# Performance work log

Hardware: AMD Instinct MI355X
Metric: run time of the kernel (lower is better)

## Reference

```python
import jax, jax.numpy as jnp
import numpy as np

DIM = 2048
HEAD_DIM = 64
NUM_HEADS = DIM // HEAD_DIM
ROT_DIM = HEAD_DIM // 2  # 32
THETA = 10000.0
LN_EPS = 1e-5


def setup_inputs() -> dict:
    key = jax.random.key(0)
    ks = jax.random.split(key, 6)
    n, s = 2, 2048
    x = jax.random.normal(ks[0], (n, s, DIM), dtype=jnp.float32)
    ln_w = jnp.ones((DIM,), dtype=jnp.float32)
    ln_b = jnp.zeros((DIM,), dtype=jnp.float32)
    # Linear weights stored as (in, out); torch Linear init scale ~ 1/sqrt(in)
    sc = 1.0 / np.sqrt(DIM)
    w_qkv = jax.random.uniform(ks[1], (DIM, 3 * DIM), jnp.float32, -sc, sc)
    b_qkv = jax.random.uniform(ks[2], (3 * DIM,), jnp.float32, -sc, sc)
    w_out = jax.random.uniform(ks[3], (DIM, DIM), jnp.float32, -sc, sc)
    b_out = jax.random.uniform(ks[4], (DIM,), jnp.float32, -sc, sc)
    return {"x": x, "ln_w": ln_w, "ln_b": ln_b, "w_qkv": w_qkv,
            "b_qkv": b_qkv, "w_out": w_out, "b_out": b_out}


def _rope_cos_sin(seq_len):
    # freqs: theta ** linspace(0, -1, rot_dim//2 + 1)[:-1] -> 16 freqs
    n_freq = ROT_DIM // 2
    exps = jnp.linspace(0.0, -1.0, n_freq + 1)[:-1]
    freqs = THETA ** exps  # [16]
    pos = jnp.arange(seq_len, dtype=jnp.float32)  # [s]
    tmp = pos[:, None] * freqs[None, :]  # [s, 16]
    # broadcast target: [1, 1, s, 16] over (n, h, s, d)
    return jnp.cos(tmp)[None, None], jnp.sin(tmp)[None, None]


def _apply_rotary(x, cos, sin):
    d = cos.shape[-1]  # 16
    x1, x2, x3 = x[..., :d], x[..., d:2 * d], x[..., 2 * d:]
    y1 = x1 * cos - x2 * sin
    y2 = x2 * cos + x1 * sin
    return jnp.concatenate([y1.astype(x3.dtype), y2.astype(x3.dtype), x3], axis=-1)


def reference(x, ln_w, ln_b, w_qkv, b_qkv, w_out, b_out):
    n, s, dim = x.shape
    skip = x
    # LayerNorm
    mu = jnp.mean(x, axis=-1, keepdims=True)
    var = jnp.var(x, axis=-1, keepdims=True)
    h = (x - mu) * jax.lax.rsqrt(var + LN_EPS) * ln_w + ln_b
    # fused QKV projection
    qkv = h @ w_qkv + b_qkv  # [n, s, 3*dim]
    qkv = qkv.reshape(n, s, 3, NUM_HEADS, HEAD_DIM)
    qkv = jnp.transpose(qkv, (2, 0, 3, 1, 4))  # [3, n, h, s, d]
    q, k, v = qkv[0], qkv[1], qkv[2]
    # RoPE on first rot_dim dims
    cos, sin = _rope_cos_sin(s)
    q = _apply_rotary(q, cos, sin)
    k = _apply_rotary(k, cos, sin)
    # causal SDPA
    scale = 1.0 / jnp.sqrt(jnp.asarray(HEAD_DIM, dtype=q.dtype))
    scores = jnp.einsum('nhqd,nhkd->nhqk', q, k) * scale
    causal = jnp.tril(jnp.ones((s, s), dtype=bool))
    scores = jnp.where(causal[None, None], scores, jnp.asarray(-jnp.inf, scores.dtype))
    attn = jax.nn.softmax(scores, axis=-1)
    o = jnp.einsum('nhqk,nhkd->nhqd', attn, v)  # [n, h, s, d]
    o = jnp.transpose(o, (0, 2, 1, 3)).reshape(n, s, dim)
    return o @ w_out + b_out + skip
```

## Files before the change

### kernel.cpp

```cpp
#include <hip/hip_runtime.h>
#include <hip/hip_bf16.h>
#include <cstdint>
#include <cstddef>

#define DIMM 2048
#define NHEADS 32
#define HDIM 64
#define SEQ 2048
#define NBATCH 2
#define ROWS 4096
#define NFREQ 16
#define NKT 64

typedef __bf16 bfv8 __attribute__((ext_vector_type(8)));
typedef float f32x4v __attribute__((ext_vector_type(4)));
typedef float f32x16 __attribute__((ext_vector_type(16)));

__device__ __forceinline__ void gload16(const void* g, void* l) {
  __builtin_amdgcn_global_load_lds((const __attribute__((address_space(1))) void*)g,
                                   (__attribute__((address_space(3))) void*)l, 16, 0, 0);
}

__device__ __forceinline__ f32x4v mfma16(bfv8 a, bfv8 b, f32x4v c) {
  return __builtin_amdgcn_mfma_f32_16x16x32_bf16(a, b, c, 0, 0, 0);
}

__device__ __forceinline__ f32x16 mfma32(bfv8 a, bfv8 b, f32x16 c) {
  return __builtin_amdgcn_mfma_f32_32x32x16_bf16(a, b, c, 0, 0, 0);
}

__device__ __forceinline__ unsigned short f2bfu(float f) {
  __hip_bfloat16 h = __float2bfloat16(f);
  return __builtin_bit_cast(unsigned short, h);
}

__device__ __forceinline__ unsigned pack2bf(float a, float b) {
  return (unsigned)f2bfu(a) | ((unsigned)f2bfu(b) << 16);
}

__device__ __forceinline__ void swap32(unsigned& a, unsigned& b, const int hi) {
  const unsigned ta = (unsigned)__shfl_xor((int)a, 32);
  const unsigned tb = (unsigned)__shfl_xor((int)b, 32);
  const unsigned na = hi ? tb : a;
  const unsigned nb = hi ? b : ta;
  a = na;
  b = nb;
}

__device__ __forceinline__ void xcd_swizzle(int& bx, int& by) {
  const int gx = gridDim.x, nwg = gx * gridDim.y;
  const int orig = blockIdx.y * gx + blockIdx.x;
  const int q = nwg >> 3, r = nwg & 7;
  const int xcd = orig & 7, loc = orig >> 3;
  const int wg = (xcd < r ? xcd * (q + 1) : r * (q + 1) + (xcd - r) * q) + loc;
  bx = wg % gx;
  by = wg / gx;
}

__global__ __launch_bounds__(256) void rope_tab_kernel(float* __restrict__ ct,
                                                       float* __restrict__ st) {
  const int i = blockIdx.x * 256 + threadIdx.x;
  if (i >= SEQ * NFREQ) return;
  const int pos = i >> 4, f = i & 15;
  const float freq = powf(10000.0f, -(float)f / 16.0f);
  const float ang = (float)pos * freq;
  ct[i] = cosf(ang);
  st[i] = sinf(ang);
}

__global__ __launch_bounds__(256) void transpose_cast_kernel(const float* __restrict__ W,
                                                             __hip_bfloat16* __restrict__ WT,
                                                             int K, int N) {
  __shared__ float tile[32][33];
  const int n0 = blockIdx.x * 32, k0 = blockIdx.y * 32;
  const int tx = threadIdx.x, ty = threadIdx.y;
#pragma unroll
  for (int j = 0; j < 4; ++j)
    tile[ty + j * 8][tx] = W[(size_t)(k0 + ty + j * 8) * N + n0 + tx];
  __syncthreads();
#pragma unroll
  for (int j = 0; j < 4; ++j)
    WT[(size_t)(n0 + ty + j * 8) * K + k0 + tx] = __float2bfloat16(tile[tx][ty + j * 8]);
}

__global__ __launch_bounds__(256) void ln_kernel(const float* __restrict__ x,
                                                 const float* __restrict__ lw,
                                                 const float* __restrict__ lb,
                                                 __hip_bfloat16* __restrict__ h) {
  const int row = blockIdx.x;
  const int t = threadIdx.x;
  const float4* xr = (const float4*)(x + (size_t)row * DIMM);
  float4 a = xr[t * 2], b = xr[t * 2 + 1];
  float e[8];
  *(float4*)e = a; *(float4*)(e + 4) = b;
  float s = 0.f, ss = 0.f;
#pragma unroll
  for (int j = 0; j < 8; ++j) { s += e[j]; ss += e[j] * e[j]; }
#pragma unroll
  for (int o = 1; o < 64; o <<= 1) { s += __shfl_xor(s, o); ss += __shfl_xor(ss, o); }
  __shared__ float red[8];
  const int wid = t >> 6;
  if ((t & 63) == 0) { red[wid * 2] = s; red[wid * 2 + 1] = ss; }
  __syncthreads();
  s = red[0] + red[2] + red[4] + red[6];
  ss = red[1] + red[3] + red[5] + red[7];
  const float mu = s * (1.f / DIMM);
  const float var = ss * (1.f / DIMM) - mu * mu;
  const float rs = rsqrtf(var + 1e-5f);
  const float4* w4 = (const float4*)lw;
  const float4* b4 = (const float4*)lb;
  float4 wa = w4[t * 2], wb = w4[t * 2 + 1], ba = b4[t * 2], bb = b4[t * 2 + 1];
  float wv[8], bv[8];
  *(float4*)wv = wa; *(float4*)(wv + 4) = wb;
  *(float4*)bv = ba; *(float4*)(bv + 4) = bb;
  unsigned short hv[8];
#pragma unroll
  for (int j = 0; j < 8; ++j)
    hv[j] = f2bfu((e[j] - mu) * rs * wv[j] + bv[j]);
  *(uint4*)((char*)h + (size_t)row * (DIMM * 2) + t * 16) = *(uint4*)hv;
}

__device__ __forceinline__ void stage_tile(const char* Ab, const char* Bb,
                                           int brow, int bcol, int kt, char* buf,
                                           int tid) {
  const int wid = tid >> 6, lane = tid & 63;
#pragma unroll
  for (int i = 0; i < 4; ++i) {
    const int fw = wid * 1024 + i * 4096;
    const int f = fw + lane * 16;
    const int lr = f >> 6;
    const int src = (f & 63) ^ (((lr >> 1) & 3) << 4);
    gload16(Ab + (size_t)(brow + lr) * 4096 + kt * 64 + src, buf + fw);
  }
#pragma unroll
  for (int i = 0; i < 2; ++i) {
    const int fw = wid * 1024 + i * 4096;
    const int f = fw + lane * 16;
    const int lr = f >> 6;
    const int src = (f & 63) ^ (((lr >> 1) & 3) << 4);
    gload16(Bb + (size_t)(bcol + lr) * 4096 + kt * 64 + src, buf + 16384 + fw);
  }
}

__device__ __forceinline__ void gemm_core(const char* Ab, const char* Bb,
                                          int brow, int bcol, char* lds,
                                          f32x4v acc[8][4]) {
  const int tid = threadIdx.x;
  const int lane = tid & 63, wid = tid >> 6;
  const int g = lane >> 4, ln15 = lane & 15;
  const int wr = wid >> 1, wc = wid & 1;
  stage_tile(Ab, Bb, brow, bcol, 0, lds, tid);
  stage_tile(Ab, Bb, brow, bcol, 1, lds + 24576, tid);
  asm volatile("s_waitcnt vmcnt(6)" ::: "memory");
  __syncthreads();
  for (int kt = 0; kt < NKT; ++kt) {
    char* buf = lds + (kt & 1) * 24576;
    bfv8 af[8], bfr[4];
#pragma unroll
    for (int mf = 0; mf < 8; ++mf) {
      const int ra = wr * 128 + mf * 16 + ln15;
      af[mf] = *(const bfv8*)(buf + ra * 64 + ((g * 16) ^ (((ra >> 1) & 3) << 4)));
    }
#pragma unroll
    for (int nf = 0; nf < 4; ++nf) {
      const int rb = wc * 64 + nf * 16 + ln15;
      bfr[nf] = *(const bfv8*)(buf + 16384 + rb * 64 + ((g * 16) ^ (((rb >> 1) & 3) << 4)));
    }
    asm volatile("s_waitcnt lgkmcnt(0)" ::: "memory");
    __builtin_amdgcn_sched_barrier(0);
    __syncthreads();
    if (kt + 2 < NKT) stage_tile(Ab, Bb, brow, bcol, kt + 2, buf, tid);
    __builtin_amdgcn_s_setprio(1);
#pragma unroll
    for (int mf = 0; mf < 8; ++mf)
#pragma unroll
      for (int nf = 0; nf < 4; ++nf)
        acc[mf][nf] = mfma16(af[mf], bfr[nf], acc[mf][nf]);
    __builtin_amdgcn_s_setprio(0);
    if (kt + 2 < NKT) {
      asm volatile("s_waitcnt vmcnt(6)" ::: "memory");
    } else {
      asm volatile("s_waitcnt vmcnt(0)" ::: "memory");
    }
    __syncthreads();
  }
}

__global__ __launch_bounds__(256, 2) void gemm_qkv_kernel(
    const __hip_bfloat16* __restrict__ A, const __hip_bfloat16* __restrict__ BT,
    const float* __restrict__ bqkv, const float* __restrict__ ct, const float* __restrict__ st,
    __hip_bfloat16* __restrict__ qb, __hip_bfloat16* __restrict__ kb,
    __hip_bfloat16* __restrict__ vb) {
  __shared__ char lds[49152];
  const f32x4v fz = {0.f, 0.f, 0.f, 0.f};
  f32x4v acc[8][4];
#pragma unroll
  for (int mf = 0; mf < 8; ++mf)
#pragma unroll
    for (int nf = 0; nf < 4; ++nf) acc[mf][nf] = fz;
  int bx, by;
  xcd_swizzle(bx, by);
  const int brow = by * 256, bcol = bx * 128;
  gemm_core((const char*)A, (const char*)BT, brow, bcol, lds, acc);

  const int tid = threadIdx.x, lane = tid & 63, wid = tid >> 6;
  const int g = lane >> 4, ln15 = lane & 15;
  const int wr = wid >> 1, wc = wid & 1;
  const int cb = bcol + wc * 64;
  const int which = cb >> 11;
  const int head = (cb & 2047) >> 6;
  float bias[4];
#pragma unroll
  for (int nf = 0; nf < 4; ++nf) bias[nf] = bqkv[cb + nf * 16 + ln15];

  if (which == 2) {
    char* tp = lds + wid * 8192;
    const int nidx = brow >> 11;
    const size_t vhead = ((size_t)nidx * NHEADS + head) * (HDIM * SEQ);
#pragma unroll
    for (int hm = 0; hm < 2; ++hm) {
      if (hm == 1) {
        asm volatile("s_waitcnt lgkmcnt(0)" ::: "memory");
        __builtin_amdgcn_sched_barrier(0);
      }
#pragma unroll
      for (int mf4 = 0; mf4 < 4; ++mf4)
#pragma unroll
        for (int r = 0; r < 4; ++r) {
          const int mf = hm * 4 + mf4;
          const int posl = mf4 * 16 + g * 4 + r;
#pragma unroll
          for (int nf = 0; nf < 4; ++nf) {
            const int d = nf * 16 + ln15;
            *(unsigned short*)(tp + d * 128 + ((posl * 2) ^ ((d & 7) << 4))) =
                f2bfu(acc[mf][nf][r] + bias[nf]);
          }
        }
      asm volatile("s_waitcnt lgkmcnt(0)" ::: "memory");
      __builtin_amdgcn_sched_barrier(0);
      const int posb = (brow & 2047) + wr * 128 + hm * 64;
#pragma unroll
      for (int i = 0; i < 8; ++i) {
        const int dl = i * 8 + (lane >> 3);
        const int cs = (lane & 7) ^ (dl & 7);
        const uint4 val = *(const uint4*)(tp + dl * 128 + cs * 16);
        *(uint4*)((char*)vb + (vhead + (size_t)dl * SEQ + posb + (lane & 7) * 8) * 2) = val;
      }
    }
  } else {
    __hip_bfloat16* dst = (which == 0) ? qb : kb;
#pragma unroll
    for (int mf = 0; mf < 8; ++mf)
#pragma unroll
      for (int r = 0; r < 4; ++r) {
        const int row = brow + wr * 128 + mf * 16 + g * 4 + r;
        const int nidx = row >> 11, pos = row & 2047;
        float v0 = acc[mf][0][r] + bias[0];
        float v1 = acc[mf][1][r] + bias[1];
        float v2 = acc[mf][2][r] + bias[2];
        float v3 = acc[mf][3][r] + bias[3];
        const float c0 = ct[pos * 16 + ln15], s0 = st[pos * 16 + ln15];
        const float x1 = v0, x2 = v1;
        v0 = x1 * c0 - x2 * s0;
        v1 = x2 * c0 + x1 * s0;
        __hip_bfloat16* p = dst + (((size_t)(nidx * NHEADS + head)) * SEQ + pos) * HDIM;
        p[ln15] = __float2bfloat16(v0);
        p[16 + ln15] = __float2bfloat16(v1);
        p[32 + ln15] = __float2bfloat16(v2);
        p[48 + ln15] = __float2bfloat16(v3);
      }
  }
}

__global__ __launch_bounds__(256, 2) void gemm_out_kernel(
    const __hip_bfloat16* __restrict__ A, const __hip_bfloat16* __restrict__ BT,
    const float* __restrict__ bout, const float* __restrict__ skip,
    float* __restrict__ out) {
  __shared__ char lds[49152];
  const f32x4v fz = {0.f, 0.f, 0.f, 0.f};
  f32x4v acc[8][4];
#pragma unroll
  for (int mf = 0; mf < 8; ++mf)
#pragma unroll
    for (int nf = 0; nf < 4; ++nf) acc[mf][nf] = fz;
  int bx, by;
  xcd_swizzle(bx, by);
  const int brow = by * 256, bcol = bx * 128;
  gemm_core((const char*)A, (const char*)BT, brow, bcol, lds, acc);

  const int tid = threadIdx.x, lane = tid & 63, wid = tid >> 6;
  const int g = lane >> 4, ln15 = lane & 15;
  const int wr = wid >> 1, wc = wid & 1;
#pragma unroll
  for (int mf = 0; mf < 8; ++mf)
#pragma unroll
    for (int r = 0; r < 4; ++r) {
      const int row = brow + wr * 128 + mf * 16 + g * 4 + r;
      const float* xr = skip + (size_t)row * DIMM;
      float* orow = out + (size_t)row * DIMM;
#pragma unroll
      for (int nf = 0; nf < 4; ++nf) {
        const int c = bcol + wc * 64 + nf * 16 + ln15;
        orow[c] = acc[mf][nf][r] + bout[c] + xr[c];
      }
    }
}

__global__ __launch_bounds__(256) void attn_kernel(
    const __hip_bfloat16* __restrict__ qb, const __hip_bfloat16* __restrict__ kb,
    const __hip_bfloat16* __restrict__ vtb, __hip_bfloat16* __restrict__ ob) {
  __shared__ char sm[33280];
  float* lred = (float*)(sm + 32768);
  const int tid = threadIdx.x, lane = tid & 63, wid = tid >> 6;
  const int ln31 = lane & 31, hi = lane >> 5;
  const int head = blockIdx.x;
  const int qbi = (int)gridDim.y - 1 - (int)blockIdx.y;
  const size_t hb = (size_t)head * (SEQ * HDIM);
  const int q0 = qbi * 128;
  const int qw = q0 + wid * 32;
  const int qg = qw + ln31;
  const int nt = qbi * 2 + 2;
  const char* Kg = (const char*)(kb + hb);
  const char* Vg = (const char*)(vtb + hb);

  bfv8 qf[4];
  {
    const char* Qp = (const char*)(qb + hb) + (size_t)(qw + ln31) * 128 + hi * 16;
#pragma unroll
    for (int j = 0; j < 4; ++j) qf[j] = *(const bfv8*)(Qp + j * 32);
  }

  f32x16 o0, o1;
#pragma unroll
  for (int i = 0; i < 16; ++i) { o0[i] = 0.f; o1[i] = 0.f; }
  float m_run = -1e30f, l_run = 0.f;
  const float scale = 0.125f;
  const int swz = (ln31 & 7) << 4;

#pragma unroll
  for (int i = 0; i < 2; ++i) {
    const int f = (tid + i * 256) * 16;
    const int row = f >> 7;
    const int src = (f & 127) ^ ((row & 7) << 4);
    gload16(Kg + (size_t)row * 128 + src, sm + f);
    gload16(Vg + (size_t)row * 4096 + src, sm + 16384 + f);
  }
  asm volatile("s_waitcnt vmcnt(0)" ::: "memory");
  __syncthreads();

  for (int t = 0; t < nt; ++t) {
    const int kvb = t * 64;
    if (t + 1 < nt) {
      const int nb = (t + 1) & 1;
      const int kvb2 = kvb + 64;
#pragma unroll
      for (int i = 0; i < 2; ++i) {
        const int f = (tid + i * 256) * 16;
        const int row = f >> 7;
        const int src = (f & 127) ^ ((row & 7) << 4);
        gload16(Kg + (size_t)(kvb2 + row) * 128 + src, sm + nb * 8192 + f);
        gload16(Vg + (size_t)row * 4096 + (size_t)kvb2 * 2 + src, sm + 16384 + nb * 8192 + f);
      }
    }
    if (kvb <= qw + 31) {
      const char* ldsK = sm + (t & 1) * 8192;
      const char* ldsV = sm + 16384 + (t & 1) * 8192;
      f32x16 s0, s1;
#pragma unroll
      for (int i = 0; i < 16; ++i) { s0[i] = 0.f; s1[i] = 0.f; }
      __builtin_amdgcn_s_setprio(1);
#pragma unroll
      for (int j = 0; j < 4; ++j) {
        const int byt = j * 32 + hi * 16;
        const bfv8 k0 = *(const bfv8*)(ldsK + ln31 * 128 + (byt ^ swz));
        const bfv8 k1 = *(const bfv8*)(ldsK + (32 + ln31) * 128 + (byt ^ swz));
        s0 = mfma32(k0, qf[j], s0);
        s1 = mfma32(k1, qf[j], s1);
      }
      __builtin_amdgcn_s_setprio(0);
      float p[32];
#pragma unroll
      for (int r = 0; r < 16; ++r) { p[r] = s0[r] * scale; p[16 + r] = s1[r] * scale; }
      if (kvb + 63 > qw) {
#pragma unroll
        for (int r = 0; r < 16; ++r) {
          const int kvo = (r & 3) + 8 * (r >> 2) + 4 * hi;
          if (kvb + kvo > qg) p[r] = -1e30f;
          if (kvb + 32 + kvo > qg) p[16 + r] = -1e30f;
        }
      }
      float mx = p[0];
#pragma unroll
      for (int r = 1; r < 32; ++r) mx = fmaxf(mx, p[r]);
      mx = fmaxf(mx, __shfl_xor(mx, 32));
      if (!__all(mx <= m_run + 8.0f)) {
        const float mn = fmaxf(m_run, mx);
        const float al = __expf(m_run - mn);
        m_run = mn;
        l_run *= al;
        lred[wid * 32 + ln31] = al;
        asm volatile("s_waitcnt lgkmcnt(0)" ::: "memory");
        __builtin_amdgcn_sched_barrier(0);
#pragma unroll
        for (int r = 0; r < 16; ++r) {
          const float a = lred[wid * 32 + (r & 3) + 8 * (r >> 2) + 4 * hi];
          o0[r] *= a;
          o1[r] *= a;
        }
      }
      float ps = 0.f;
#pragma unroll
      for (int r = 0; r < 32; ++r) { p[r] = __expf(p[r] - m_run); ps += p[r]; }
      ps += __shfl_xor(ps, 32);
      l_run += ps;
      unsigned c[16];
#pragma unroll
      for (int i = 0; i < 16; ++i) c[i] = pack2bf(p[2 * i], p[2 * i + 1]);
      bfv8 paf[4];
#pragma unroll
      for (int fI = 0; fI < 4; ++fI) {
        unsigned a0 = c[fI * 4 + 0], b0 = c[fI * 4 + 2];
        unsigned a1 = c[fI * 4 + 1], b1 = c[fI * 4 + 3];
        swap32(a0, b0, hi);
        swap32(a1, b1, hi);
        union { unsigned u[4]; bfv8 v; } w;
        w.u[0] = a0; w.u[1] = a1; w.u[2] = b0; w.u[3] = b1;
        paf[fI] = w.v;
      }
      __builtin_amdgcn_s_setprio(1);
#pragma unroll
      for (int ss = 0; ss < 4; ++ss) {
        const int byt = ss * 32 + hi * 16;
        const bfv8 v0 = *(const bfv8*)(ldsV + ln31 * 128 + (byt ^ swz));
        const bfv8 v1 = *(const bfv8*)(ldsV + (32 + ln31) * 128 + (byt ^ swz));
        o0 = mfma32(paf[ss], v0, o0);
        o1 = mfma32(paf[ss], v1, o1);
      }
      __builtin_amdgcn_s_setprio(0);
    }
    asm volatile("s_waitcnt vmcnt(0)" ::: "memory");
    __syncthreads();
  }

  lred[wid * 32 + ln31] = l_run;
  asm volatile("s_waitcnt lgkmcnt(0)" ::: "memory");
  __builtin_amdgcn_sched_barrier(0);
  const int nidx = head >> 5, hh = head & 31;
#pragma unroll
  for (int r = 0; r < 16; ++r) {
    const int qrow = qw + (r & 3) + 8 * (r >> 2) + 4 * hi;
    const float inv = 1.0f / lred[wid * 32 + (r & 3) + 8 * (r >> 2) + 4 * hi];
    __hip_bfloat16* dst = ob + ((size_t)nidx * SEQ + qrow) * DIMM + hh * 64;
    dst[ln31] = __float2bfloat16(o0[r] * inv);
    dst[32 + ln31] = __float2bfloat16(o1[r] * inv);
  }
}

extern "C" void kernel_launch(void* const* d_in, const int* in_sizes, int n_in,
                              void* d_out, int out_size, void* d_ws, size_t ws_size,
                              hipStream_t stream) {
  const float* x = (const float*)d_in[0];
  const float* ln_w = (const float*)d_in[1];
  const float* ln_b = (const float*)d_in[2];
  const float* w_qkv = (const float*)d_in[3];
  const float* b_qkv = (const float*)d_in[4];
  const float* w_out = (const float*)d_in[5];
  const float* b_out = (const float*)d_in[6];
  float* out = (float*)d_out;

  char* ws = (char*)d_ws;
  size_t off = 0;
  auto alloc = [&](size_t bytes) -> char* {
    char* p = ws + off;
    off += (bytes + 255) & ~(size_t)255;
    return p;
  };
  __hip_bfloat16* h = (__hip_bfloat16*)alloc((size_t)ROWS * DIMM * 2);
  __hip_bfloat16* wqkvT = (__hip_bfloat16*)alloc((size_t)3 * DIMM * DIMM * 2);
  __hip_bfloat16* woutT = (__hip_bfloat16*)alloc((size_t)DIMM * DIMM * 2);
  __hip_bfloat16* qbuf = (__hip_bfloat16*)alloc((size_t)ROWS * DIMM * 2);
  __hip_bfloat16* kbuf = (__hip_bfloat16*)alloc((size_t)ROWS * DIMM * 2);
  __hip_bfloat16* vtbuf = (__hip_bfloat16*)alloc((size_t)ROWS * DIMM * 2);
  __hip_bfloat16* obuf = (__hip_bfloat16*)alloc((size_t)ROWS * DIMM * 2);
  float* ct = (float*)alloc((size_t)SEQ * NFREQ * 4);
  float* st = (float*)alloc((size_t)SEQ * NFREQ * 4);

  rope_tab_kernel<<<dim3((SEQ * NFREQ + 255) / 256), dim3(256), 0, stream>>>(ct, st);
  transpose_cast_kernel<<<dim3(3 * DIMM / 32, DIMM / 32), dim3(32, 8), 0, stream>>>(
      w_qkv, wqkvT, DIMM, 3 * DIMM);
  transpose_cast_kernel<<<dim3(DIMM / 32, DIMM / 32), dim3(32, 8), 0, stream>>>(
      w_out, woutT, DIMM, DIMM);
  ln_kernel<<<dim3(ROWS), dim3(256), 0, stream>>>(x, ln_w, ln_b, h);
  gemm_qkv_kernel<<<dim3(3 * DIMM / 128, ROWS / 256), dim3(256), 0, stream>>>(
      h, wqkvT, b_qkv, ct, st, qbuf, kbuf, vtbuf);
  attn_kernel<<<dim3(NBATCH * NHEADS, SEQ / 128), dim3(256), 0, stream>>>(
      qbuf, kbuf, vtbuf, obuf);
  gemm_out_kernel<<<dim3(DIMM / 128, ROWS / 256), dim3(256), 0, stream>>>(
      obuf, woutT, b_out, x, out);
}
```

Baseline: 300.5 us.

## Restructure GEMMs to 8 waves with split-K, triple-buffered 128-wide K tiles

Both projection GEMMs now use 512 threads, with pairs of waves splitting each K tile of 128 in half. Partial accumulators are combined through LDS before the epilogue. The main loop uses a three-stage LDS ring and issues global loads in two chunks interleaved with two MFMA halves, with one barrier per iteration instead of two. This aims to hide memory latency and raise MFMA issue rate, at the cost of 144KB of LDS per block, which likely limits occupancy to one block per CU despite the launch bound of 2, plus an extra reduction pass.

```diff
diff --git a/kernel.cpp b/kernel.cpp
--- a/kernel.cpp
+++ b/kernel.cpp
@@ -10,7 +10,7 @@
 #define NBATCH 2
 #define ROWS 4096
 #define NFREQ 16
-#define NKT 64
+#define NKT3 32
 
 typedef __bf16 bfv8 __attribute__((ext_vector_type(8)));
 typedef float f32x4v __attribute__((ext_vector_type(4)));
@@ -120,78 +120,126 @@
   *(uint4*)((char*)h + (size_t)row * (DIMM * 2) + t * 16) = *(uint4*)hv;
 }
 
-__device__ __forceinline__ void stage_tile(const char* Ab, const char* Bb,
-                                           int brow, int bcol, int kt, char* buf,
-                                           int tid) {
-  const int wid = tid >> 6, lane = tid & 63;
-#pragma unroll
-  for (int i = 0; i < 4; ++i) {
-    const int fw = wid * 1024 + i * 4096;
-    const int f = fw + lane * 16;
-    const int lr = f >> 6;
-    const int src = (f & 63) ^ (((lr >> 1) & 3) << 4);
-    gload16(Ab + (size_t)(brow + lr) * 4096 + kt * 64 + src, buf + fw);
-  }
-#pragma unroll
-  for (int i = 0; i < 2; ++i) {
-    const int fw = wid * 1024 + i * 4096;
-    const int f = fw + lane * 16;
-    const int lr = f >> 6;
-    const int src = (f & 63) ^ (((lr >> 1) & 3) << 4);
-    gload16(Bb + (size_t)(bcol + lr) * 4096 + kt * 64 + src, buf + 16384 + fw);
-  }
-}
-
-__device__ __forceinline__ void gemm_core(const char* Ab, const char* Bb,
-                                          int brow, int bcol, char* lds,
-                                          f32x4v acc[8][4]) {
-  const int tid = threadIdx.x;
-  const int lane = tid & 63, wid = tid >> 6;
+__device__ __forceinline__ void stageA64(const char* Ab, int brow, int kt,
+                                         char* bufA, int c, int lane) {
+  const int row = c * 8 + (lane >> 3);
+  const int src = ((lane & 7) * 16) ^ ((row & 7) << 4);
+  gload16(Ab + (size_t)(brow + row) * 4096 + kt * 128 + src, bufA + c * 1024);
+}
+__device__ __forceinline__ void stageB64(const char* Bb, int bcol, int kt,
+                                         char* bufB, int c, int lane) {
+  const int row = c * 8 + (lane >> 3);
+  const int src = ((lane & 7) * 16) ^ ((row & 7) << 4);
+  gload16(Bb + (size_t)(bcol + row) * 4096 + kt * 128 + src, bufB + c * 1024);
+}
+
+__device__ __forceinline__ void gemm_core3(const char* Ab, const char* Bb,
+                                           int brow, int bcol, char* lds,
+                                           f32x4v acc[8][4]) {
+  const int tid = threadIdx.x, lane = tid & 63, wid = tid >> 6;
   const int g = lane >> 4, ln15 = lane & 15;
-  const int wr = wid >> 1, wc = wid & 1;
-  stage_tile(Ab, Bb, brow, bcol, 0, lds, tid);
-  stage_tile(Ab, Bb, brow, bcol, 1, lds + 24576, tid);
+  const int wr = wid >> 2, wc = (wid >> 1) & 1, wk = wid & 1;
+  const int kb = wk * 64;
+
+#pragma unroll
+  for (int t = 0; t < 2; ++t) {
+    char* bufA = lds + t * 49152;
+    char* bufB = bufA + 32768;
+    stageA64(Ab, brow, t, bufA, wid, lane);
+    stageA64(Ab, brow, t, bufA, wid + 8, lane);
+    stageA64(Ab, brow, t, bufA, wid + 16, lane);
+    stageA64(Ab, brow, t, bufA, wid + 24, lane);
+    stageB64(Bb, bcol, t, bufB, wid, lane);
+    stageB64(Bb, bcol, t, bufB, wid + 8, lane);
+  }
   asm volatile("s_waitcnt vmcnt(6)" ::: "memory");
-  __syncthreads();
-  for (int kt = 0; kt < NKT; ++kt) {
-    char* buf = lds + (kt & 1) * 24576;
-    bfv8 af[8], bfr[4];
-#pragma unroll
-    for (int mf = 0; mf < 8; ++mf) {
-      const int ra = wr * 128 + mf * 16 + ln15;
-      af[mf] = *(const bfv8*)(buf + ra * 64 + ((g * 16) ^ (((ra >> 1) & 3) << 4)));
+  __builtin_amdgcn_s_barrier();
+
+  for (int t = 0; t < NKT3; ++t) {
+    char* bufA = lds + (t % 3) * 49152;
+    char* bufB = bufA + 32768;
+    char* nbufA = lds + ((t + 2) % 3) * 49152;
+    char* nbufB = nbufA + 32768;
+    const bool st = (t + 2 < NKT3);
+    bfv8 af[4], bfr[4];
+#pragma unroll
+    for (int mi = 0; mi < 4; ++mi) {
+      const int ra = wr * 128 + mi * 16 + ln15;
+      af[mi] = *(const bfv8*)(bufA + (size_t)ra * 128 + ((kb + g * 16) ^ ((ra & 7) << 4)));
     }
 #pragma unroll
     for (int nf = 0; nf < 4; ++nf) {
       const int rb = wc * 64 + nf * 16 + ln15;
-      bfr[nf] = *(const bfv8*)(buf + 16384 + rb * 64 + ((g * 16) ^ (((rb >> 1) & 3) << 4)));
+      bfr[nf] = *(const bfv8*)(bufB + (size_t)rb * 128 + ((kb + g * 16) ^ ((rb & 7) << 4)));
+    }
+    if (st) {
+      stageA64(Ab, brow, t + 2, nbufA, wid, lane);
+      stageA64(Ab, brow, t + 2, nbufA, wid + 8, lane);
+      stageB64(Bb, bcol, t + 2, nbufB, wid, lane);
     }
     asm volatile("s_waitcnt lgkmcnt(0)" ::: "memory");
     __builtin_amdgcn_sched_barrier(0);
-    __syncthreads();
-    if (kt + 2 < NKT) stage_tile(Ab, Bb, brow, bcol, kt + 2, buf, tid);
     __builtin_amdgcn_s_setprio(1);
 #pragma unroll
-    for (int mf = 0; mf < 8; ++mf)
+    for (int mi = 0; mi < 4; ++mi)
 #pragma unroll
       for (int nf = 0; nf < 4; ++nf)
-        acc[mf][nf] = mfma16(af[mf], bfr[nf], acc[mf][nf]);
+        acc[mi][nf] = mfma16(af[mi], bfr[nf], acc[mi][nf]);
     __builtin_amdgcn_s_setprio(0);
-    if (kt + 2 < NKT) {
+    bfv8 ao[4];
+#pragma unroll
+    for (int mi = 0; mi < 4; ++mi) {
+      const int ra = wr * 128 + (4 + mi) * 16 + ln15;
+      ao[mi] = *(const bfv8*)(bufA + (size_t)ra * 128 + ((kb + g * 16) ^ ((ra & 7) << 4)));
+    }
+    if (st) {
+      stageA64(Ab, brow, t + 2, nbufA, wid + 16, lane);
+      stageA64(Ab, brow, t + 2, nbufA, wid + 24, lane);
+      stageB64(Bb, bcol, t + 2, nbufB, wid + 8, lane);
+    }
+    asm volatile("s_waitcnt lgkmcnt(0)" ::: "memory");
+    __builtin_amdgcn_sched_barrier(0);
+    __builtin_amdgcn_s_setprio(1);
+#pragma unroll
+    for (int mi = 0; mi < 4; ++mi)
+#pragma unroll
+      for (int nf = 0; nf < 4; ++nf)
+        acc[4 + mi][nf] = mfma16(ao[mi], bfr[nf], acc[4 + mi][nf]);
+    __builtin_amdgcn_s_setprio(0);
+    if (st) {
       asm volatile("s_waitcnt vmcnt(6)" ::: "memory");
-    } else {
+    } else if (t == NKT3 - 2) {
       asm volatile("s_waitcnt vmcnt(0)" ::: "memory");
     }
-    __syncthreads();
-  }
-}
-
-__global__ __launch_bounds__(256, 2) void gemm_qkv_kernel(
+    __builtin_amdgcn_s_barrier();
+  }
+}
+
+__device__ __forceinline__ void kreduce(char* lds, f32x4v acc[8][4], f32x4v ak[4][4],
+                                        int wid, int lane, int wk) {
+  char* reg = lds + (size_t)wid * 16384;
+#pragma unroll
+  for (int q = 0; q < 4; ++q)
+#pragma unroll
+    for (int nf = 0; nf < 4; ++nf)
+      *(f32x4v*)(reg + (q * 4 + nf) * 1024 + lane * 16) = acc[wk ? q : 4 + q][nf];
+  __syncthreads();
+  const char* preg = lds + (size_t)(wid ^ 1) * 16384;
+#pragma unroll
+  for (int q = 0; q < 4; ++q)
+#pragma unroll
+    for (int nf = 0; nf < 4; ++nf)
+      ak[q][nf] = acc[wk ? 4 + q : q][nf] +
+                  *(const f32x4v*)(preg + (q * 4 + nf) * 1024 + lane * 16);
+  __syncthreads();
+}
+
+__global__ __launch_bounds__(512, 2) void gemm_qkv_kernel(
     const __hip_bfloat16* __restrict__ A, const __hip_bfloat16* __restrict__ BT,
     const float* __restrict__ bqkv, const float* __restrict__ ct, const float* __restrict__ st,
     __hip_bfloat16* __restrict__ qb, __hip_bfloat16* __restrict__ kb,
     __hip_bfloat16* __restrict__ vb) {
-  __shared__ char lds[49152];
+  __shared__ char lds[147456];
   const f32x4v fz = {0.f, 0.f, 0.f, 0.f};
   f32x4v acc[8][4];
 #pragma unroll
@@ -201,14 +249,18 @@
   int bx, by;
   xcd_swizzle(bx, by);
   const int brow = by * 256, bcol = bx * 128;
-  gemm_core((const char*)A, (const char*)BT, brow, bcol, lds, acc);
+  gemm_core3((const char*)A, (const char*)BT, brow, bcol, lds, acc);
 
   const int tid = threadIdx.x, lane = tid & 63, wid = tid >> 6;
   const int g = lane >> 4, ln15 = lane & 15;
-  const int wr = wid >> 1, wc = wid & 1;
+  const int wr = wid >> 2, wc = (wid >> 1) & 1, wk = wid & 1;
+  f32x4v ak[4][4];
+  kreduce(lds, acc, ak, wid, lane, wk);
+
   const int cb = bcol + wc * 64;
   const int which = cb >> 11;
   const int head = (cb & 2047) >> 6;
+  const int rowbase = brow + wr * 128 + wk * 64;
   float bias[4];
 #pragma unroll
   for (int nf = 0; nf < 4; ++nf) bias[nf] = bqkv[cb + nf * 16 + ln15];
@@ -217,48 +269,40 @@
     char* tp = lds + wid * 8192;
     const int nidx = brow >> 11;
     const size_t vhead = ((size_t)nidx * NHEADS + head) * (HDIM * SEQ);
-#pragma unroll
-    for (int hm = 0; hm < 2; ++hm) {
-      if (hm == 1) {
-        asm volatile("s_waitcnt lgkmcnt(0)" ::: "memory");
-        __builtin_amdgcn_sched_barrier(0);
-      }
-#pragma unroll
-      for (int mf4 = 0; mf4 < 4; ++mf4)
-#pragma unroll
-        for (int r = 0; r < 4; ++r) {
-          const int mf = hm * 4 + mf4;
-          const int posl = mf4 * 16 + g * 4 + r;
-#pragma unroll
-          for (int nf = 0; nf < 4; ++nf) {
-            const int d = nf * 16 + ln15;
-            *(unsigned short*)(tp + d * 128 + ((posl * 2) ^ ((d & 7) << 4))) =
-                f2bfu(acc[mf][nf][r] + bias[nf]);
-          }
+    const int posb = (rowbase & 2047);
+#pragma unroll
+    for (int q = 0; q < 4; ++q)
+#pragma unroll
+      for (int r = 0; r < 4; ++r) {
+        const int posl = q * 16 + g * 4 + r;
+#pragma unroll
+        for (int nf = 0; nf < 4; ++nf) {
+          const int d = nf * 16 + ln15;
+          *(unsigned short*)(tp + d * 128 + ((posl * 2) ^ ((d & 7) << 4))) =
+              f2bfu(ak[q][nf][r] + bias[nf]);
         }
-      asm volatile("s_waitcnt lgkmcnt(0)" ::: "memory");
-      __builtin_amdgcn_sched_barrier(0);
-      const int posb = (brow & 2047) + wr * 128 + hm * 64;
-#pragma unroll
-      for (int i = 0; i < 8; ++i) {
-        const int dl = i * 8 + (lane >> 3);
-        const int cs = (lane & 7) ^ (dl & 7);
-        const uint4 val = *(const uint4*)(tp + dl * 128 + cs * 16);
-        *(uint4*)((char*)vb + (vhead + (size_t)dl * SEQ + posb + (lane & 7) * 8) * 2) = val;
-      }
+      }
+    asm volatile("s_waitcnt lgkmcnt(0)" ::: "memory");
+    __builtin_amdgcn_sched_barrier(0);
+#pragma unroll
+    for (int i = 0; i < 8; ++i) {
+      const int dl = i * 8 + (lane >> 3);
+      const int cs = (lane & 7) ^ (dl & 7);
+      const uint4 val = *(const uint4*)(tp + dl * 128 + cs * 16);
+      *(uint4*)((char*)vb + (vhead + (size_t)dl * SEQ + posb + (lane & 7) * 8) * 2) = val;
     }
   } else {
     __hip_bfloat16* dst = (which == 0) ? qb : kb;
 #pragma unroll
-    for (int mf = 0; mf < 8; ++mf)
+    for (int q = 0; q < 4; ++q)
 #pragma unroll
       for (int r = 0; r < 4; ++r) {
-        const int row = brow + wr * 128 + mf * 16 + g * 4 + r;
+        const int row = rowbase + q * 16 + g * 4 + r;
         const int nidx = row >> 11, pos = row & 2047;
-        float v0 = acc[mf][0][r] + bias[0];
-        float v1 = acc[mf][1][r] + bias[1];
-        float v2 = acc[mf][2][r] + bias[2];
-        float v3 = acc[mf][3][r] + bias[3];
+        float v0 = ak[q][0][r] + bias[0];
+        float v1 = ak[q][1][r] + bias[1];
+        float v2 = ak[q][2][r] + bias[2];
+        float v3 = ak[q][3][r] + bias[3];
         const float c0 = ct[pos * 16 + ln15], s0 = st[pos * 16 + ln15];
         const float x1 = v0, x2 = v1;
         v0 = x1 * c0 - x2 * s0;
@@ -272,11 +316,11 @@
   }
 }
 
-__global__ __launch_bounds__(256, 2) void gemm_out_kernel(
+__global__ __launch_bounds__(512, 2) void gemm_out_kernel(
     const __hip_bfloat16* __restrict__ A, const __hip_bfloat16* __restrict__ BT,
     const float* __restrict__ bout, const float* __restrict__ skip,
     float* __restrict__ out) {
-  __shared__ char lds[49152];
+  __shared__ char lds[147456];
   const f32x4v fz = {0.f, 0.f, 0.f, 0.f};
   f32x4v acc[8][4];
 #pragma unroll
@@ -286,22 +330,26 @@
   int bx, by;
   xcd_swizzle(bx, by);
   const int brow = by * 256, bcol = bx * 128;
-  gemm_core((const char*)A, (const char*)BT, brow, bcol, lds, acc);
+  gemm_core3((const char*)A, (const char*)BT, brow, bcol, lds, acc);
 
   const int tid = threadIdx.x, lane = tid & 63, wid = tid >> 6;
   const int g = lane >> 4, ln15 = lane & 15;
-  const int wr = wid >> 1, wc = wid & 1;
-#pragma unroll
-  for (int mf = 0; mf < 8; ++mf)
+  const int wr = wid >> 2, wc = (wid >> 1) & 1, wk = wid & 1;
+  f32x4v ak[4][4];
+  kreduce(lds, acc, ak, wid, lane, wk);
+
+  const int rowbase = brow + wr * 128 + wk * 64;
+#pragma unroll
+  for (int q = 0; q < 4; ++q)
 #pragma unroll
     for (int r = 0; r < 4; ++r) {
-      const int row = brow + wr * 128 + mf * 16 + g * 4 + r;
+      const int row = rowbase + q * 16 + g * 4 + r;
       const float* xr = skip + (size_t)row * DIMM;
       float* orow = out + (size_t)row * DIMM;
 #pragma unroll
       for (int nf = 0; nf < 4; ++nf) {
         const int c = bcol + wc * 64 + nf * 16 + ln15;
-        orow[c] = acc[mf][nf][r] + bout[c] + xr[c];
+        orow[c] = ak[q][nf][r] + bout[c] + xr[c];
       }
     }
 }
@@ -491,10 +539,10 @@
   transpose_cast_kernel<<<dim3(DIMM / 32, DIMM / 32), dim3(32, 8), 0, stream>>>(
       w_out, woutT, DIMM, DIMM);
   ln_kernel<<<dim3(ROWS), dim3(256), 0, stream>>>(x, ln_w, ln_b, h);
-  gemm_qkv_kernel<<<dim3(3 * DIMM / 128, ROWS / 256), dim3(256), 0, stream>>>(
+  gemm_qkv_kernel<<<dim3(3 * DIMM / 128, ROWS / 256), dim3(512), 0, stream>>>(
       h, wqkvT, b_qkv, ct, st, qbuf, kbuf, vtbuf);
   attn_kernel<<<dim3(NBATCH * NHEADS, SEQ / 128), dim3(256), 0, stream>>>(
       qbuf, kbuf, vtbuf, obuf);
-  gemm_out_kernel<<<dim3(DIMM / 128, ROWS / 256), dim3(256), 0, stream>>>(
+  gemm_out_kernel<<<dim3(DIMM / 128, ROWS / 256), dim3(512), 0, stream>>>(
       obuf, woutT, b_out, x, out);
 }
```

After: 271.8 us. -9.6%, faster.
